# Kernel tuning notes

Measured on AMD Instinct MI355X. Metric: run time of the kernel, lower is better.

Reference implementation:

```python
import jax, jax.numpy as jnp
import numpy as np

B, P, ENC = 128, 625, 512
A, E, H, V = 256, 256, 512, 70
START_TOK, END_TOK = 68, 69


def setup_inputs() -> dict:
    key = jax.random.key(0)
    ks = jax.random.split(key, 20)
    w = lambda k, shape: jax.random.normal(k, shape, jnp.float32) * 0.02
    return {
        "encoder_out": jax.random.normal(ks[0], (B, P, ENC), jnp.float32),
        "emb": w(ks[1], (V, E)),
        "We": w(ks[2], (ENC, A)), "be": jnp.zeros((A,), jnp.float32),
        "Wd": w(ks[3], (H, A)),   "bd": jnp.zeros((A,), jnp.float32),
        "wf": w(ks[4], (A,)),     "bf": jnp.zeros((), jnp.float32),
        "Wh0": w(ks[5], (ENC, H)), "bh0": jnp.zeros((H,), jnp.float32),
        "Wc0": w(ks[6], (ENC, H)), "bc0": jnp.zeros((H,), jnp.float32),
        "Wb": w(ks[7], (H, ENC)), "bb": jnp.zeros((ENC,), jnp.float32),
        "Wih": w(ks[8], (E + ENC, 4 * H)), "Whh": w(ks[9], (H, 4 * H)),
        "bih": jnp.zeros((4 * H,), jnp.float32), "bhh": jnp.zeros((4 * H,), jnp.float32),
        "Wfc": w(ks[10], (H, V)), "bfc": jnp.zeros((V,), jnp.float32),
        "decode_lengths": 70,
    }


def _decode(encoder_out, emb, We, be, Wd, bd, wf, bf, Wh0, bh0, Wc0, bc0,
            Wb, bb, Wih, Whh, bih, bhh, Wfc, bfc, decode_lengths):
    enc = encoder_out  # [B, P, ENC]
    batch = enc.shape[0]
    # encoder_att projection is constant across timesteps -> hoist out of loop
    att1 = enc @ We + be                      # [B, P, A]
    mean_enc = enc.mean(axis=1)               # [B, ENC]
    h0 = mean_enc @ Wh0 + bh0                 # [B, H]
    c0 = mean_enc @ Wc0 + bc0                 # [B, H]
    emb0 = emb[jnp.full((batch,), START_TOK)]  # [B, E]
    lstm_b = bih + bhh

    def step(carry, _):
        h, c, emb_t, done = carry
        att2 = h @ Wd + bd                                            # [B, A]
        e = jnp.einsum('bpa,a->bp', jax.nn.relu(att1 + att2[:, None, :]), wf) + bf
        alpha = jax.nn.softmax(e, axis=1)                             # [B, P]
        awe = jnp.einsum('bp,bpe->be', alpha, enc)                    # [B, ENC]
        awe = jax.nn.sigmoid(h @ Wb + bb) * awe                       # gated
        gates = jnp.concatenate([emb_t, awe], axis=1) @ Wih + h @ Whh + lstm_b
        i_, f_, g_, o_ = jnp.split(gates, 4, axis=1)                  # torch order i,f,g,o
        c_new = jax.nn.sigmoid(f_) * c + jax.nn.sigmoid(i_) * jnp.tanh(g_)
        h_new = jax.nn.sigmoid(o_) * jnp.tanh(c_new)
        preds = h_new @ Wfc + bfc                                     # [B, V] (dropout eval = id)
        preds_out = jnp.where(done, 0.0, preds)                       # zeros after early break
        done_new = done | (jnp.argmax(preds) == END_TOK)              # flat argmax, as in torch
        emb_new = emb[jnp.argmax(preds, axis=-1)]                     # greedy feedback
        return (h_new, c_new, emb_new, done_new), preds_out

    init = (h0, c0, emb0, jnp.array(False))
    _, preds_seq = jax.lax.scan(step, init, None, length=decode_lengths)
    return jnp.transpose(preds_seq, (1, 0, 2))  # [B, T, V]


def reference(encoder_out, emb, We, be, Wd, bd, wf, bf, Wh0, bh0, Wc0, bc0,
              Wb, bb, Wih, Whh, bih, bhh, Wfc, bfc, decode_lengths):
    return _decode(encoder_out, emb, We, be, Wd, bd, wf, bf, Wh0, bh0, Wc0, bc0,
                   Wb, bb, Wih, Whh, bih, bhh, Wfc, bfc, decode_lengths)
```

## Files before the change

### kernel.cpp

```cpp
#include <hip/hip_runtime.h>
#include <math.h>

#define Bn 128
#define Pn 625
#define ENCn 512
#define An 256
#define En 256
#define Hn 512
#define Vn 70
#define G4n 2048
#define STARTT 68
#define ENDT 69
#define NCHUNK 10
#define PCH 63
#define PSTRIDE 520
#define KSPLIT 16
#define KCH 80


__global__ __launch_bounds__(256) void k_mean(const float* __restrict__ enc,
                                              float* __restrict__ mean_enc) {
  int b = blockIdx.x, t = threadIdx.x;
  const float* e = enc + (size_t)b * Pn * ENCn;
  float s0 = 0.f, s1 = 0.f;
  for (int p = 0; p < Pn; ++p) {
    s0 += e[(size_t)p * ENCn + t];
    s1 += e[(size_t)p * ENCn + t + 256];
  }
  mean_enc[b * ENCn + t] = s0 * (1.0f / 625.0f);
  mean_enc[b * ENCn + t + 256] = s1 * (1.0f / 625.0f);
}

__global__ __launch_bounds__(256) void k_prep(const float* __restrict__ Wfc,
                                              float* __restrict__ WfcT) {
  int j = blockIdx.x * 256 + threadIdx.x;
  if (j < Hn * Vn) {
    int k = j / Vn, vv = j - k * Vn;
    WfcT[(size_t)vv * Hn + k] = Wfc[j];
  }
}

__global__ __launch_bounds__(512) void k_init(const float* __restrict__ mean_enc,
                       const float* __restrict__ Wh0, const float* __restrict__ bh0,
                       const float* __restrict__ Wc0, const float* __restrict__ bc0,
                       const float* __restrict__ emb,
                       float* __restrict__ h0, float* __restrict__ c0,
                       float* __restrict__ emb_t, int* __restrict__ done_arr) {
  int b = blockIdx.x, t = threadIdx.x;
  const float* W = blockIdx.y ? Wc0 : Wh0;
  const float* bias = blockIdx.y ? bc0 : bh0;
  float* out = blockIdx.y ? c0 : h0;
  __shared__ float ms[ENCn];
  ms[t] = mean_enc[b * ENCn + t];
  __syncthreads();
  float s = bias[t];
  for (int k = 0; k < ENCn; ++k) s += ms[k] * W[k * Hn + t];
  out[b * Hn + t] = s;
  if (blockIdx.y == 0 && t < En) emb_t[b * En + t] = emb[STARTT * En + t];
  if (blockIdx.y == 0 && b == 0 && t == 0) done_arr[0] = 0;
}

__global__ __launch_bounds__(256) void k_att1(const float* __restrict__ Am,
                       const float* __restrict__ We,
                       const float* __restrict__ be, float* __restrict__ att1) {
  __shared__ float sA[16][128];
  __shared__ float sB[16][128];
  int n0 = blockIdx.x * 128, m0 = blockIdx.y * 128;
  int t = threadIdx.x;
  int tm = (t >> 4) * 8, tn = (t & 15) * 8;
  float acc[8][8];
#pragma unroll
  for (int i = 0; i < 8; ++i)
#pragma unroll
    for (int j = 0; j < 8; ++j) acc[i][j] = 0.f;
  for (int k0 = 0; k0 < 512; k0 += 16) {
    __syncthreads();
#pragma unroll
    for (int i = 0; i < 8; ++i) {
      int idx = t + i * 256;
      int mm = idx >> 4, kk = idx & 15;
      sA[kk][mm] = Am[(size_t)(m0 + mm) * 512 + k0 + kk];
      int kk2 = idx >> 7, nn = idx & 127;
      sB[kk2][nn] = We[(size_t)(k0 + kk2) * 256 + n0 + nn];
    }
    __syncthreads();
#pragma unroll
    for (int kk = 0; kk < 16; ++kk) {
      float a[8], bq[8];
      *(float4*)&a[0] = *(const float4*)&sA[kk][tm];
      *(float4*)&a[4] = *(const float4*)&sA[kk][tm + 4];
      *(float4*)&bq[0] = *(const float4*)&sB[kk][tn];
      *(float4*)&bq[4] = *(const float4*)&sB[kk][tn + 4];
#pragma unroll
      for (int i = 0; i < 8; ++i)
#pragma unroll
        for (int j = 0; j < 8; ++j) acc[i][j] += a[i] * bq[j];
    }
  }
  float ber[8];
  *(float4*)&ber[0] = *(const float4*)&be[n0 + tn];
  *(float4*)&ber[4] = *(const float4*)&be[n0 + tn + 4];
#pragma unroll
  for (int i = 0; i < 8; ++i) {
    float o[8];
#pragma unroll
    for (int j = 0; j < 8; ++j) o[j] = acc[i][j] + ber[j];
    *(float4*)&att1[(size_t)(m0 + tm + i) * An + n0 + tn] = *(float4*)&o[0];
    *(float4*)&att1[(size_t)(m0 + tm + i) * An + n0 + tn + 4] = *(float4*)&o[4];
  }
}


__global__ __launch_bounds__(256) void k_proj(const float* __restrict__ h,
                       const float* __restrict__ Wd, const float* __restrict__ bd,
                       const float* __restrict__ Wb, const float* __restrict__ bbv,
                       float* __restrict__ att2, float* __restrict__ gate,
                       const float* __restrict__ preds,
                       const int* __restrict__ done_prev, int* __restrict__ done_cur,
                       int do_flat) {
  int t = threadIdx.x;
  if (blockIdx.x == Bn) {
    if (blockIdx.y != 0 || !do_flat) return;
    __shared__ float sv[256];
    __shared__ int si[256];
    float bv = -1e30f; int bi = 0x7fffffff;
    for (int i = t; i < Bn * Vn; i += 256) {
      float v = preds[i];
      if (v > bv) { bv = v; bi = i; }
    }
    sv[t] = bv; si[t] = bi;
    __syncthreads();
    for (int s = 128; s > 0; s >>= 1) {
      if (t < s) {
        if (sv[t + s] > sv[t] || (sv[t + s] == sv[t] && si[t + s] < si[t])) {
          sv[t] = sv[t + s]; si[t] = si[t + s];
        }
      }
      __syncthreads();
    }
    if (t == 0) *done_cur = (*done_prev) | (si[0] == ENDT ? 1 : 0);
    return;
  }
  int b = blockIdx.x;
  __shared__ float hsh[Hn];
  hsh[t] = h[b * Hn + t];
  hsh[t + 256] = h[b * Hn + t + 256];
  __syncthreads();
  if (blockIdx.y == 0) {
    float s0 = bd[t];
    float s1 = bbv[t];
    for (int k = 0; k < Hn; ++k) {
      float hv = hsh[k];
      s0 += hv * Wd[(size_t)k * An + t];
      s1 += hv * Wb[(size_t)k * ENCn + t];
    }
    att2[b * An + t] = s0;
    gate[b * ENCn + t] = 1.f / (1.f + expf(-s1));
  } else {
    float s2 = bbv[t + 256];
    for (int k = 0; k < Hn; ++k) s2 += hsh[k] * Wb[(size_t)k * ENCn + t + 256];
    gate[b * ENCn + t + 256] = 1.f / (1.f + expf(-s2));
  }
}

__global__ __launch_bounds__(256) void k_attn(const float* __restrict__ att1,
                       const float* __restrict__ att2,
                       const float* __restrict__ wf, const float* __restrict__ bfp,
                       const float* __restrict__ enc, float* __restrict__ part) {
  int c = blockIdx.x, b = blockIdx.y, t = threadIdx.x;
  int lane = t & 63, wv = t >> 6;
  int p0 = c * PCH;
  int n = Pn - p0; if (n > PCH) n = PCH;
  __shared__ float es[PCH];
  __shared__ float red[256];
  float4 a2 = ((const float4*)(att2 + b * An))[lane];
  float4 wfr = ((const float4*)wf)[lane];
  float bfv = *bfp;
  const float* a1b = att1 + ((size_t)b * Pn + p0) * An;
  for (int p = wv; p < n; p += 4) {
    float4 v = ((const float4*)(a1b + (size_t)p * An))[lane];
    float s = fmaxf(v.x + a2.x, 0.f) * wfr.x
            + fmaxf(v.y + a2.y, 0.f) * wfr.y
            + fmaxf(v.z + a2.z, 0.f) * wfr.z
            + fmaxf(v.w + a2.w, 0.f) * wfr.w;
    for (int o = 32; o > 0; o >>= 1) s += __shfl_down(s, o, 64);
    if (lane == 0) es[p] = s + bfv;
  }
  __syncthreads();
  float m = (t < n) ? es[t] : -1e30f;
  red[t] = m;
  __syncthreads();
  for (int s = 128; s > 0; s >>= 1) {
    if (t < s) red[t] = fmaxf(red[t], red[t + s]);
    __syncthreads();
  }
  m = red[0];
  __syncthreads();
  float lp = 0.f;
  if (t < n) {
    float e2 = expf(es[t] - m);
    es[t] = e2;
    lp = e2;
  }
  red[t] = lp;
  __syncthreads();
  for (int s = 128; s > 0; s >>= 1) {
    if (t < s) red[t] += red[t + s];
    __syncthreads();
  }
  float l = red[0];
  float acc0 = 0.f, acc1 = 0.f;
  const float* ebase = enc + ((size_t)b * Pn + p0) * ENCn;
  int p = 0;
#pragma unroll 4
  for (; p + 1 < n; p += 2) {
    float wp0 = es[p], wp1 = es[p + 1];
    float2 ev0 = ((const float2*)(ebase + (size_t)p * ENCn))[t];
    float2 ev1 = ((const float2*)(ebase + (size_t)(p + 1) * ENCn))[t];
    acc0 += wp0 * ev0.x;
    acc1 += wp0 * ev0.y;
    acc0 += wp1 * ev1.x;
    acc1 += wp1 * ev1.y;
  }
  if (p < n) {
    float wp = es[p];
    float2 ev = ((const float2*)(ebase + (size_t)p * ENCn))[t];
    acc0 += wp * ev.x;
    acc1 += wp * ev.y;
  }
  float* pp = part + (size_t)(b * NCHUNK + c) * PSTRIDE;
  if (t == 0) { pp[0] = m; pp[1] = l; }
  *(float2*)&pp[8 + 2 * t] = make_float2(acc0, acc1);
}

__global__ __launch_bounds__(256) void k_combine(const float* __restrict__ part,
                       const float* __restrict__ gate, float* __restrict__ awe) {
  int b = blockIdx.x, col = blockIdx.y * 256 + threadIdx.x;
  const float* pb = part + (size_t)b * NCHUNK * PSTRIDE;
  float M = -1e30f;
#pragma unroll
  for (int c = 0; c < NCHUNK; ++c) M = fmaxf(M, pb[c * PSTRIDE]);
  float L = 0.f, sc[NCHUNK];
#pragma unroll
  for (int c = 0; c < NCHUNK; ++c) {
    float s = expf(pb[c * PSTRIDE] - M);
    sc[c] = s;
    L += s * pb[c * PSTRIDE + 1];
  }
  float inv = 1.f / L;
  float a = 0.f;
#pragma unroll
  for (int c = 0; c < NCHUNK; ++c) a += sc[c] * pb[c * PSTRIDE + 8 + col];
  awe[b * ENCn + col] = a * inv * gate[b * ENCn + col];
}

__global__ __launch_bounds__(256) void k_gates(const float* __restrict__ embt,
                       const float* __restrict__ awe, const float* __restrict__ h,
                       const float* __restrict__ Wih, const float* __restrict__ Whh,
                       float* __restrict__ gp) {
  int n0 = blockIdx.x * 64;
  int sI = blockIdx.y;
  int k0 = sI * KCH;
  int t = threadIdx.x;
  int tc = t & 15, tg = t >> 4;
  int nc = n0 + tc * 4;
  float4 acc[8];
#pragma unroll
  for (int r = 0; r < 8; ++r) acc[r] = make_float4(0.f, 0.f, 0.f, 0.f);
  for (int kk = 0; kk < KCH; kk += 4) {
    int k = k0 + kk;
    const float* wbase = (k < 768) ? (Wih + (size_t)k * G4n + nc)
                                   : (Whh + (size_t)(k - 768) * G4n + nc);
    float4 w0 = *(const float4*)(wbase);
    float4 w1 = *(const float4*)(wbase + G4n);
    float4 w2 = *(const float4*)(wbase + 2 * G4n);
    float4 w3 = *(const float4*)(wbase + 3 * G4n);
#pragma unroll
    for (int r = 0; r < 8; ++r) {
      int row = tg * 8 + r;
      float4 xv;
      if (k < 256)      xv = *(const float4*)(embt + row * En + k);
      else if (k < 768) xv = *(const float4*)(awe + row * ENCn + (k - 256));
      else              xv = *(const float4*)(h + row * Hn + (k - 768));
      acc[r].x += xv.x * w0.x + xv.y * w1.x + xv.z * w2.x + xv.w * w3.x;
      acc[r].y += xv.x * w0.y + xv.y * w1.y + xv.z * w2.y + xv.w * w3.y;
      acc[r].z += xv.x * w0.z + xv.y * w1.z + xv.z * w2.z + xv.w * w3.z;
      acc[r].w += xv.x * w0.w + xv.y * w1.w + xv.z * w2.w + xv.w * w3.w;
    }
  }
#pragma unroll
  for (int r = 0; r < 8; ++r)
    *(float4*)(gp + ((size_t)sI * Bn + tg * 8 + r) * G4n + nc) = acc[r];
}

__global__ __launch_bounds__(512) void k_lstm(const float* __restrict__ gp,
                       const float* __restrict__ bih, const float* __restrict__ bhh,
                       const float* __restrict__ c_in, float* __restrict__ c_out,
                       float* __restrict__ h_out,
                       const float* __restrict__ WfcT, const float* __restrict__ bfc,
                       const float* __restrict__ emb, float* __restrict__ preds,
                       float* __restrict__ emb_next, float* __restrict__ out,
                       const int* __restrict__ done_t, int step, int T) {
  int b = blockIdx.x, t = threadIdx.x;
  float gi = bih[t] + bhh[t];
  float gf = bih[t + 512] + bhh[t + 512];
  float gg = bih[t + 1024] + bhh[t + 1024];
  float go = bih[t + 1536] + bhh[t + 1536];
  for (int s = 0; s < KSPLIT; ++s) {
    const float* row = gp + ((size_t)s * Bn + b) * G4n;
    gi += row[t];
    gf += row[t + 512];
    gg += row[t + 1024];
    go += row[t + 1536];
  }
  float cv = (1.f / (1.f + expf(-gf))) * c_in[b * Hn + t]
           + (1.f / (1.f + expf(-gi))) * tanhf(gg);
  float hv = (1.f / (1.f + expf(-go))) * tanhf(cv);
  c_out[b * Hn + t] = cv;
  h_out[b * Hn + t] = hv;
  __shared__ float hs[Hn];
  __shared__ float ps[Vn];
  __shared__ int tokS;
  hs[t] = hv;
  __syncthreads();
  int lane = t & 63, wvi = t >> 6;
  for (int v = wvi; v < Vn; v += 8) {
    float s = 0.f;
    for (int k = lane; k < Hn; k += 64) s += hs[k] * WfcT[(size_t)v * Hn + k];
    for (int o = 32; o > 0; o >>= 1) s += __shfl_down(s, o, 64);
    if (lane == 0) ps[v] = s + bfc[v];
  }
  __syncthreads();
  int done = *done_t;
  if (t < Vn) {
    float pv = ps[t];
    preds[b * Vn + t] = pv;
    out[((size_t)b * T + step) * Vn + t] = done ? 0.f : pv;
  }
  if (t == 0) {
    float bv = ps[0]; int bi = 0;
    for (int v = 1; v < Vn; ++v)
      if (ps[v] > bv) { bv = ps[v]; bi = v; }
    tokS = bi;
  }
  __syncthreads();
  if (t < En) emb_next[b * En + t] = emb[tokS * En + t];
}


extern "C" void kernel_launch(void* const* d_in, const int* in_sizes, int n_in,
                              void* d_out, int out_size, void* d_ws, size_t ws_size,
                              hipStream_t stream) {
  const float* enc = (const float*)d_in[0];
  const float* emb = (const float*)d_in[1];
  const float* We  = (const float*)d_in[2];
  const float* be  = (const float*)d_in[3];
  const float* Wd  = (const float*)d_in[4];
  const float* bd  = (const float*)d_in[5];
  const float* wf  = (const float*)d_in[6];
  const float* bf  = (const float*)d_in[7];
  const float* Wh0 = (const float*)d_in[8];
  const float* bh0 = (const float*)d_in[9];
  const float* Wc0 = (const float*)d_in[10];
  const float* bc0 = (const float*)d_in[11];
  const float* Wb  = (const float*)d_in[12];
  const float* bb  = (const float*)d_in[13];
  const float* Wih = (const float*)d_in[14];
  const float* Whh = (const float*)d_in[15];
  const float* bih = (const float*)d_in[16];
  const float* bhh = (const float*)d_in[17];
  const float* Wfc = (const float*)d_in[18];
  const float* bfc = (const float*)d_in[19];
  int T = out_size / (Bn * Vn);

  float* w = (float*)d_ws;
  size_t off = 0;
  float* att1 = w + off;     off += (size_t)Bn * Pn * An;
  float* WfcT = w + off;     off += (size_t)Hn * Vn;
  float* mean_enc = w + off; off += Bn * ENCn;
  float* hb0 = w + off;      off += Bn * Hn;
  float* hb1 = w + off;      off += Bn * Hn;
  float* cb0 = w + off;      off += Bn * Hn;
  float* cb1 = w + off;      off += Bn * Hn;
  float* eb0 = w + off;      off += Bn * En;
  float* eb1 = w + off;      off += Bn * En;
  float* att2 = w + off;     off += Bn * An;
  float* gate = w + off;     off += Bn * ENCn;
  float* part = w + off;     off += (size_t)Bn * NCHUNK * PSTRIDE;
  float* awe = w + off;      off += Bn * ENCn;
  float* gatesP = w + off;   off += (size_t)KSPLIT * Bn * G4n;
  float* preds = w + off;    off += Bn * Vn;
  off = (off + 255) & ~(size_t)255;
  int* done_arr = (int*)(w + off);

  float* hbuf[2] = {hb0, hb1};
  float* cbuf[2] = {cb0, cb1};
  float* ebuf[2] = {eb0, eb1};

  k_mean<<<Bn, 256, 0, stream>>>(enc, mean_enc);
  k_prep<<<(Hn * Vn + 255) / 256, 256, 0, stream>>>(Wfc, WfcT);
  k_init<<<dim3(Bn, 2), 512, 0, stream>>>(mean_enc, Wh0, bh0, Wc0, bc0, emb,
                                          hb0, cb0, eb0, done_arr);
  k_att1<<<dim3(2, 625), 256, 0, stream>>>(enc, We, be, att1);

  int cur = 0;
  for (int t = 0; t < T; ++t) {
    int nxt = cur ^ 1;
    k_proj<<<dim3(Bn + 1, 2), 256, 0, stream>>>(hbuf[cur], Wd, bd, Wb, bb, att2, gate, preds,
                                       done_arr + (t > 0 ? t - 1 : 0), done_arr + t,
                                       t > 0 ? 1 : 0);
    k_attn<<<dim3(NCHUNK, Bn), 256, 0, stream>>>(att1, att2, wf, bf, enc, part);
    k_combine<<<dim3(Bn, 2), 256, 0, stream>>>(part, gate, awe);
    k_gates<<<dim3(32, KSPLIT), 256, 0, stream>>>(ebuf[cur], awe, hbuf[cur], Wih, Whh, gatesP);
    k_lstm<<<Bn, 512, 0, stream>>>(gatesP, bih, bhh, cbuf[cur], cbuf[nxt], hbuf[nxt],
                                   WfcT, bfc, emb, preds, ebuf[nxt], (float*)d_out,
                                   done_arr + t, t, T);
    cur = nxt;
  }
}
```

Baseline: 8.367 ms.

## Move output projection and greedy feedback into next step's projection kernel

The vocabulary projection, argmax token selection and embedding lookup move out of the LSTM kernel into the y=1 blocks of the next step's k_proj, which were previously doing less work. The LSTM cell kernel is split into 2x128 blocks of 256 threads for more parallelism. The flat-argmax done-flag reduction moves into k_combine, and a final kernel emits the last step's predictions. The intent is to shorten the serial per-step critical path and balance load across blocks. In exchange, the done flag and output for each step are now written one step later, which makes the ordering more intricate.

```diff
diff --git a/kernel.cpp b/kernel.cpp
--- a/kernel.cpp
+++ b/kernel.cpp
@@ -114,35 +114,17 @@
 __global__ __launch_bounds__(256) void k_proj(const float* __restrict__ h,
                        const float* __restrict__ Wd, const float* __restrict__ bd,
                        const float* __restrict__ Wb, const float* __restrict__ bbv,
+                       const float* __restrict__ WfcT, const float* __restrict__ bfc,
+                       const float* __restrict__ emb,
                        float* __restrict__ att2, float* __restrict__ gate,
-                       const float* __restrict__ preds,
-                       const int* __restrict__ done_prev, int* __restrict__ done_cur,
-                       int do_flat) {
+                       float* __restrict__ preds, float* __restrict__ embt,
+                       float* __restrict__ out, const int* __restrict__ done_arr,
+                       int step, int T) {
   int t = threadIdx.x;
-  if (blockIdx.x == Bn) {
-    if (blockIdx.y != 0 || !do_flat) return;
-    __shared__ float sv[256];
-    __shared__ int si[256];
-    float bv = -1e30f; int bi = 0x7fffffff;
-    for (int i = t; i < Bn * Vn; i += 256) {
-      float v = preds[i];
-      if (v > bv) { bv = v; bi = i; }
-    }
-    sv[t] = bv; si[t] = bi;
-    __syncthreads();
-    for (int s = 128; s > 0; s >>= 1) {
-      if (t < s) {
-        if (sv[t + s] > sv[t] || (sv[t + s] == sv[t] && si[t + s] < si[t])) {
-          sv[t] = sv[t + s]; si[t] = si[t + s];
-        }
-      }
-      __syncthreads();
-    }
-    if (t == 0) *done_cur = (*done_prev) | (si[0] == ENDT ? 1 : 0);
-    return;
-  }
   int b = blockIdx.x;
   __shared__ float hsh[Hn];
+  __shared__ float ps[Vn];
+  __shared__ int tokS;
   hsh[t] = h[b * Hn + t];
   hsh[t + 256] = h[b * Hn + t + 256];
   __syncthreads();
@@ -160,6 +142,30 @@
     float s2 = bbv[t + 256];
     for (int k = 0; k < Hn; ++k) s2 += hsh[k] * Wb[(size_t)k * ENCn + t + 256];
     gate[b * ENCn + t + 256] = 1.f / (1.f + expf(-s2));
+    if (step > 0) {
+      int lane = t & 63, wv = t >> 6;
+      for (int v = wv; v < Vn; v += 4) {
+        float s = 0.f;
+        for (int k = lane; k < Hn; k += 64) s += hsh[k] * WfcT[(size_t)v * Hn + k];
+        for (int o = 32; o > 0; o >>= 1) s += __shfl_down(s, o, 64);
+        if (lane == 0) ps[v] = s + bfc[v];
+      }
+      __syncthreads();
+      int done = done_arr[step - 1];
+      if (t < Vn) {
+        float pv = ps[t];
+        preds[b * Vn + t] = pv;
+        out[((size_t)b * T + (step - 1)) * Vn + t] = done ? 0.f : pv;
+      }
+      if (t == 0) {
+        float bv = ps[0]; int bi = 0;
+        for (int v = 1; v < Vn; ++v)
+          if (ps[v] > bv) { bv = ps[v]; bi = v; }
+        tokS = bi;
+      }
+      __syncthreads();
+      embt[b * En + t] = emb[tokS * En + t];
+    }
   }
 }
 
@@ -234,8 +240,33 @@
 }
 
 __global__ __launch_bounds__(256) void k_combine(const float* __restrict__ part,
-                       const float* __restrict__ gate, float* __restrict__ awe) {
-  int b = blockIdx.x, col = blockIdx.y * 256 + threadIdx.x;
+                       const float* __restrict__ gate, float* __restrict__ awe,
+                       const float* __restrict__ preds, int* __restrict__ done_arr,
+                       int step) {
+  int t = threadIdx.x;
+  if (blockIdx.x == Bn) {
+    if (blockIdx.y != 0 || step == 0) return;
+    __shared__ float sv[256];
+    __shared__ int si[256];
+    float bv = -1e30f; int bi = 0x7fffffff;
+    for (int i = t; i < Bn * Vn; i += 256) {
+      float v = preds[i];
+      if (v > bv) { bv = v; bi = i; }
+    }
+    sv[t] = bv; si[t] = bi;
+    __syncthreads();
+    for (int s = 128; s > 0; s >>= 1) {
+      if (t < s) {
+        if (sv[t + s] > sv[t] || (sv[t + s] == sv[t] && si[t + s] < si[t])) {
+          sv[t] = sv[t + s]; si[t] = si[t + s];
+        }
+      }
+      __syncthreads();
+    }
+    if (t == 0) done_arr[step] = done_arr[step - 1] | (si[0] == ENDT ? 1 : 0);
+    return;
+  }
+  int b = blockIdx.x, col = blockIdx.y * 256 + t;
   const float* pb = part + (size_t)b * NCHUNK * PSTRIDE;
   float M = -1e30f;
 #pragma unroll
@@ -293,58 +324,49 @@
     *(float4*)(gp + ((size_t)sI * Bn + tg * 8 + r) * G4n + nc) = acc[r];
 }
 
-__global__ __launch_bounds__(512) void k_lstm(const float* __restrict__ gp,
+__global__ __launch_bounds__(256) void k_lstm(const float* __restrict__ gp,
                        const float* __restrict__ bih, const float* __restrict__ bhh,
                        const float* __restrict__ c_in, float* __restrict__ c_out,
-                       float* __restrict__ h_out,
-                       const float* __restrict__ WfcT, const float* __restrict__ bfc,
-                       const float* __restrict__ emb, float* __restrict__ preds,
-                       float* __restrict__ emb_next, float* __restrict__ out,
-                       const int* __restrict__ done_t, int step, int T) {
-  int b = blockIdx.x, t = threadIdx.x;
-  float gi = bih[t] + bhh[t];
-  float gf = bih[t + 512] + bhh[t + 512];
-  float gg = bih[t + 1024] + bhh[t + 1024];
-  float go = bih[t + 1536] + bhh[t + 1536];
+                       float* __restrict__ h_out) {
+  int b = blockIdx.x, col = blockIdx.y * 256 + threadIdx.x;
+  float gi = bih[col] + bhh[col];
+  float gf = bih[col + 512] + bhh[col + 512];
+  float gg = bih[col + 1024] + bhh[col + 1024];
+  float go = bih[col + 1536] + bhh[col + 1536];
   for (int s = 0; s < KSPLIT; ++s) {
     const float* row = gp + ((size_t)s * Bn + b) * G4n;
-    gi += row[t];
-    gf += row[t + 512];
-    gg += row[t + 1024];
-    go += row[t + 1536];
-  }
-  float cv = (1.f / (1.f + expf(-gf))) * c_in[b * Hn + t]
+    gi += row[col];
+    gf += row[col + 512];
+    gg += row[col + 1024];
+    go += row[col + 1536];
+  }
+  float cv = (1.f / (1.f + expf(-gf))) * c_in[b * Hn + col]
            + (1.f / (1.f + expf(-gi))) * tanhf(gg);
   float hv = (1.f / (1.f + expf(-go))) * tanhf(cv);
-  c_out[b * Hn + t] = cv;
-  h_out[b * Hn + t] = hv;
-  __shared__ float hs[Hn];
+  c_out[b * Hn + col] = cv;
+  h_out[b * Hn + col] = hv;
+}
+
+__global__ __launch_bounds__(256) void k_final(const float* __restrict__ h,
+                       const float* __restrict__ WfcT, const float* __restrict__ bfc,
+                       float* __restrict__ out, const int* __restrict__ done_arr,
+                       int T) {
+  int b = blockIdx.x, t = threadIdx.x;
+  __shared__ float hsh[Hn];
   __shared__ float ps[Vn];
-  __shared__ int tokS;
-  hs[t] = hv;
-  __syncthreads();
-  int lane = t & 63, wvi = t >> 6;
-  for (int v = wvi; v < Vn; v += 8) {
+  hsh[t] = h[b * Hn + t];
+  hsh[t + 256] = h[b * Hn + t + 256];
+  __syncthreads();
+  int lane = t & 63, wv = t >> 6;
+  for (int v = wv; v < Vn; v += 4) {
     float s = 0.f;
-    for (int k = lane; k < Hn; k += 64) s += hs[k] * WfcT[(size_t)v * Hn + k];
+    for (int k = lane; k < Hn; k += 64) s += hsh[k] * WfcT[(size_t)v * Hn + k];
     for (int o = 32; o > 0; o >>= 1) s += __shfl_down(s, o, 64);
     if (lane == 0) ps[v] = s + bfc[v];
   }
   __syncthreads();
-  int done = *done_t;
-  if (t < Vn) {
-    float pv = ps[t];
-    preds[b * Vn + t] = pv;
-    out[((size_t)b * T + step) * Vn + t] = done ? 0.f : pv;
-  }
-  if (t == 0) {
-    float bv = ps[0]; int bi = 0;
-    for (int v = 1; v < Vn; ++v)
-      if (ps[v] > bv) { bv = ps[v]; bi = v; }
-    tokS = bi;
-  }
-  __syncthreads();
-  if (t < En) emb_next[b * En + t] = emb[tokS * En + t];
+  int done = done_arr[T - 1];
+  if (t < Vn) out[((size_t)b * T + (T - 1)) * Vn + t] = done ? 0.f : ps[t];
 }
 
 
@@ -382,8 +404,7 @@
   float* hb1 = w + off;      off += Bn * Hn;
   float* cb0 = w + off;      off += Bn * Hn;
   float* cb1 = w + off;      off += Bn * Hn;
-  float* eb0 = w + off;      off += Bn * En;
-  float* eb1 = w + off;      off += Bn * En;
+  float* ebuf = w + off;     off += Bn * En;
   float* att2 = w + off;     off += Bn * An;
   float* gate = w + off;     off += Bn * ENCn;
   float* part = w + off;     off += (size_t)Bn * NCHUNK * PSTRIDE;
@@ -395,26 +416,27 @@
 
   float* hbuf[2] = {hb0, hb1};
   float* cbuf[2] = {cb0, cb1};
-  float* ebuf[2] = {eb0, eb1};
 
   k_mean<<<Bn, 256, 0, stream>>>(enc, mean_enc);
   k_prep<<<(Hn * Vn + 255) / 256, 256, 0, stream>>>(Wfc, WfcT);
   k_init<<<dim3(Bn, 2), 512, 0, stream>>>(mean_enc, Wh0, bh0, Wc0, bc0, emb,
-                                          hb0, cb0, eb0, done_arr);
+                                          hb0, cb0, ebuf, done_arr);
   k_att1<<<dim3(2, 625), 256, 0, stream>>>(enc, We, be, att1);
 
   int cur = 0;
   for (int t = 0; t < T; ++t) {
     int nxt = cur ^ 1;
-    k_proj<<<dim3(Bn + 1, 2), 256, 0, stream>>>(hbuf[cur], Wd, bd, Wb, bb, att2, gate, preds,
-                                       done_arr + (t > 0 ? t - 1 : 0), done_arr + t,
-                                       t > 0 ? 1 : 0);
+    k_proj<<<dim3(Bn, 2), 256, 0, stream>>>(hbuf[cur], Wd, bd, Wb, bb,
+                                            WfcT, bfc, emb,
+                                            att2, gate, preds, ebuf,
+                                            (float*)d_out, done_arr, t, T);
     k_attn<<<dim3(NCHUNK, Bn), 256, 0, stream>>>(att1, att2, wf, bf, enc, part);
-    k_combine<<<dim3(Bn, 2), 256, 0, stream>>>(part, gate, awe);
-    k_gates<<<dim3(32, KSPLIT), 256, 0, stream>>>(ebuf[cur], awe, hbuf[cur], Wih, Whh, gatesP);
-    k_lstm<<<Bn, 512, 0, stream>>>(gatesP, bih, bhh, cbuf[cur], cbuf[nxt], hbuf[nxt],
-                                   WfcT, bfc, emb, preds, ebuf[nxt], (float*)d_out,
-                                   done_arr + t, t, T);
+    k_combine<<<dim3(Bn + 1, 2), 256, 0, stream>>>(part, gate, awe, preds,
+                                                   done_arr, t);
+    k_gates<<<dim3(32, KSPLIT), 256, 0, stream>>>(ebuf, awe, hbuf[cur], Wih, Whh, gatesP);
+    k_lstm<<<dim3(Bn, 2), 256, 0, stream>>>(gatesP, bih, bhh, cbuf[cur], cbuf[nxt],
+                                            hbuf[nxt]);
     cur = nxt;
   }
-}
+  k_final<<<Bn, 256, 0, stream>>>(hbuf[cur], WfcT, bfc, (float*)d_out, done_arr, T);
+}
```

New measurement: 8.637 ms. 1.03x slower.
